# Optimization experiments

Hardware: AMD Instinct MI355X
Metric: run time of the kernel (lower is better)

## Reference

```python
import jax, jax.numpy as jnp
import numpy as np

HIDDEN = 1024
HEADS = 16
HEAD_DIM = HIDDEN // HEADS
LN_EPS = 1e-6


def setup_inputs() -> dict:
    key = jax.random.key(0)
    ks = jax.random.split(key, 12)
    B, S, H = 2, 2048, HIDDEN
    s = 1.0 / np.sqrt(H)
    inp = {
        "hidden_states": jax.random.normal(ks[0], (B, S, H), dtype=jnp.float32),
        "attention_mask": jnp.ones((B, S), dtype=jnp.int32),
        "Wq": jax.random.normal(ks[1], (H, H), dtype=jnp.float32) * s,
        "bq": jax.random.normal(ks[2], (H,), dtype=jnp.float32) * 0.02,
        "Wk": jax.random.normal(ks[3], (H, H), dtype=jnp.float32) * s,
        "bk": jax.random.normal(ks[4], (H,), dtype=jnp.float32) * 0.02,
        "Wv": jax.random.normal(ks[5], (H, H), dtype=jnp.float32) * s,
        "bv": jax.random.normal(ks[6], (H,), dtype=jnp.float32) * 0.02,
        "Wo": jax.random.normal(ks[7], (H, H), dtype=jnp.float32) * s,
        "bo": jax.random.normal(ks[8], (H,), dtype=jnp.float32) * 0.02,
        "ln_g": jnp.ones((H,), dtype=jnp.float32),
        "ln_b": jnp.zeros((H,), dtype=jnp.float32),
    }
    return inp


def _split_heads(x):
    B, S, H = x.shape
    return x.reshape(B, S, HEADS, HEAD_DIM).transpose(0, 2, 1, 3)  # [B,h,S,d]


def reference(hidden_states, attention_mask, Wq, bq, Wk, bk, Wv, bv, Wo, bo, ln_g, ln_b):
    # torch nn.Linear: y = x @ W.T + b
    q = _split_heads(hidden_states @ Wq.T + bq)
    k = _split_heads(hidden_states @ Wk.T + bk)
    v = _split_heads(hidden_states @ Wv.T + bv)

    scores = jnp.einsum("bhqd,bhkd->bhqk", q, k) / np.sqrt(HEAD_DIM)
    # 2D mask path: [B,K] -> [B,1,1,K]; (1-mask)*-1e18 additive bias
    bias = (1.0 - attention_mask[:, None, None, :].astype(scores.dtype)) * -1e18
    probs = jax.nn.softmax(scores + bias, axis=-1)
    # dropout is identity in eval mode
    ctx = jnp.einsum("bhqk,bhkd->bhqd", probs, v)
    B, h, S, d = ctx.shape
    ctx = ctx.transpose(0, 2, 1, 3).reshape(B, S, h * d)

    out = ctx @ Wo.T + bo
    res = out + hidden_states
    mu = jnp.mean(res, axis=-1, keepdims=True)
    var = jnp.mean(jnp.square(res - mu), axis=-1, keepdims=True)
    return (res - mu) * jax.lax.rsqrt(var + LN_EPS) * ln_g + ln_b
```

## Files before the change

kernel.cpp:

```cpp
#include <hip/hip_runtime.h>
#include <hip/hip_bf16.h>

#define SEQ     2048
#define BATCH   2
#define HID     1024
#define NHEADS  16
#define HD      64
#define MTOT    4096
#define KVHALF  1024
#define LNEPS   1e-6f
#define L2E     1.4426950408889634f
#define SHIFT2  26.0f

typedef __bf16 bf16_t;
typedef bf16_t bf16x8 __attribute__((ext_vector_type(8)));
typedef bf16_t bf16x4 __attribute__((ext_vector_type(4)));
typedef short  short4v __attribute__((ext_vector_type(4)));
typedef float  floatx4 __attribute__((ext_vector_type(4)));

__device__ __forceinline__ floatx4 mfma16(bf16x8 a, bf16x8 b, floatx4 c) {
    return __builtin_amdgcn_mfma_f32_16x16x32_bf16(a, b, c, 0, 0, 0);
}
__device__ __forceinline__ floatx4 mfma16k16(bf16x4 a, bf16x4 b, floatx4 c) {
    short4v as = __builtin_bit_cast(short4v, a);
    short4v bs = __builtin_bit_cast(short4v, b);
    return __builtin_amdgcn_mfma_f32_16x16x16bf16_1k(as, bs, c, 0, 0, 0);
}
__device__ __forceinline__ bf16x8 ldg8(const bf16_t* p) { return *(const bf16x8*)p; }

__device__ __forceinline__ void glds16(const bf16_t* src, char* dst) {
    __builtin_amdgcn_global_load_lds(
        (const __attribute__((address_space(1))) unsigned int*)src,
        (__attribute__((address_space(3))) unsigned int*)dst, 16, 0, 0);
}

__device__ __forceinline__ void stage128x32(const bf16_t* __restrict__ g, int row_stride,
                                            int k0, bf16_t* lds, int wave, int lane)
{
#pragma unroll
    for (int j = 0; j < 2; j++) {
        const int rbase = wave * 32 + j * 16;
        const bf16_t* src = g + (size_t)(rbase + (lane >> 2)) * row_stride + k0 + (lane & 3) * 8;
        bf16_t* dst = lds + rbase * 32;
        __builtin_amdgcn_global_load_lds(
            (const __attribute__((address_space(1))) unsigned int*)src,
            (__attribute__((address_space(3))) unsigned int*)dst, 16, 0, 0);
    }
}
__device__ __forceinline__ void stage64x32(const bf16_t* __restrict__ g, int row_stride,
                                           int k0, bf16_t* lds, int wave, int lane)
{
    const int rbase = wave * 16;
    const bf16_t* src = g + (size_t)(rbase + (lane >> 2)) * row_stride + k0 + (lane & 3) * 8;
    bf16_t* dst = lds + rbase * 32;
    __builtin_amdgcn_global_load_lds(
        (const __attribute__((address_space(1))) unsigned int*)src,
        (__attribute__((address_space(3))) unsigned int*)dst, 16, 0, 0);
}

__global__ __launch_bounds__(256) void cvt_kernel(
    const float* sX, const float* sWq, const float* sWk, const float* sWv, const float* sWo,
    bf16_t* dX, bf16_t* dWq, bf16_t* dWk, bf16_t* dWv, bf16_t* dWo)
{
    const int z = blockIdx.z;
    const float* src; bf16_t* dst; int n;
    switch (z) {
        case 0:  src = sX;  dst = dX;  n = MTOT * HID; break;
        case 1:  src = sWq; dst = dWq; n = HID * HID;  break;
        case 2:  src = sWk; dst = dWk; n = HID * HID;  break;
        case 3:  src = sWv; dst = dWv; n = HID * HID;  break;
        default: src = sWo; dst = dWo; n = HID * HID;  break;
    }
    const int n4 = n >> 2;
    const int stride = gridDim.x * blockDim.x;
    for (int i = blockIdx.x * blockDim.x + threadIdx.x; i < n4; i += stride) {
        const float4 v = ((const float4*)src)[i];
        bf16_t o[4] = {(bf16_t)v.x, (bf16_t)v.y, (bf16_t)v.z, (bf16_t)v.w};
        *(unsigned long long*)(dst + 4 * i) = *(unsigned long long*)o;
    }
}

__global__ __launch_bounds__(256) void qkv_kernel(
    const bf16_t* __restrict__ X,
    const bf16_t* __restrict__ Wq, const float* __restrict__ bq,
    const bf16_t* __restrict__ Wk, const float* __restrict__ bk,
    const bf16_t* __restrict__ Wv, const float* __restrict__ bv,
    bf16_t* __restrict__ Qo, bf16_t* __restrict__ Ko, bf16_t* __restrict__ Vo)
{
    const int z = blockIdx.z;
    const bf16_t* W    = (z == 0) ? Wq : (z == 1) ? Wk : Wv;
    const float*  bias = (z == 0) ? bq : (z == 1) ? bk : bv;
    bf16_t*       out  = (z == 0) ? Qo : (z == 1) ? Ko : Vo;

    const int tid  = threadIdx.x;
    const int lane = tid & 63;
    const int wave = tid >> 6;
    const int l16  = lane & 15;
    const int quad = lane >> 4;
    const int m_blk = blockIdx.y * 128;
    const int n_blk = blockIdx.x * 128;
    const int m_w = (wave >> 1) * 64;
    const int n_w = (wave & 1) * 64;

    __shared__ __align__(16) char smem[18432];
    bf16_t* As = (bf16_t*)smem;
    bf16_t* Bs = (bf16_t*)(smem + 8192);

    floatx4 acc[4][4];
#pragma unroll
    for (int i = 0; i < 4; i++)
#pragma unroll
        for (int j = 0; j < 4; j++) acc[i][j] = (floatx4)0.0f;

    for (int k0 = 0; k0 < HID; k0 += 32) {
        __syncthreads();
        stage128x32(X + (size_t)m_blk * HID, HID, k0, As, wave, lane);
        stage128x32(W + (size_t)n_blk * HID, HID, k0, Bs, wave, lane);
        __syncthreads();

        bf16x8 a[4], b[4];
#pragma unroll
        for (int i = 0; i < 4; i++) a[i] = *(const bf16x8*)&As[(m_w + i * 16 + l16) * 32 + quad * 8];
#pragma unroll
        for (int j = 0; j < 4; j++) b[j] = *(const bf16x8*)&Bs[(n_w + j * 16 + l16) * 32 + quad * 8];
#pragma unroll
        for (int i = 0; i < 4; i++)
#pragma unroll
            for (int j = 0; j < 4; j++) acc[i][j] = mfma16(a[i], b[j], acc[i][j]);
    }
    __syncthreads();

    float bv_[4];
#pragma unroll
    for (int j = 0; j < 4; j++) bv_[j] = bias[n_blk + n_w + j * 16 + l16];

    bf16_t* Tw = (bf16_t*)(smem + wave * 4608);

    if (z != 2) {
        const float scale = (z == 0) ? 0.125f : 1.0f;
        const int hN = (n_blk + n_w) >> 6;
#pragma unroll
        for (int ih = 0; ih < 2; ih++) {
#pragma unroll
            for (int i2 = 0; i2 < 2; i2++) {
                const int i = ih * 2 + i2;
#pragma unroll
                for (int j = 0; j < 4; j++)
#pragma unroll
                    for (int r = 0; r < 4; r++)
                        Tw[(i2 * 16 + quad * 4 + r) * 72 + j * 16 + l16] =
                            (bf16_t)((acc[i][j][r] + bv_[j]) * scale);
            }
#pragma unroll
            for (int p = 0; p < 4; p++) {
                const int srow = p * 8 + (lane >> 3);
                const int col  = (lane & 7) * 8;
                bf16x8 v = *(const bf16x8*)&Tw[srow * 72 + col];
                const int m = m_blk + m_w + ih * 32 + srow;
                const int bb = m >> 11, s = m & (SEQ - 1);
                *(bf16x8*)&out[(((size_t)(bb * NHEADS + hN)) * SEQ + s) * HD + col] = v;
            }
        }
    } else {
        const int m0 = m_blk + m_w;
        const int bb = m0 >> 11, s0 = m0 & (SEQ - 1);
#pragma unroll
        for (int jh = 0; jh < 2; jh++) {
#pragma unroll
            for (int j2 = 0; j2 < 2; j2++) {
                const int j = jh * 2 + j2;
#pragma unroll
                for (int i = 0; i < 4; i++) {
                    bf16x4 pk;
#pragma unroll
                    for (int r = 0; r < 4; r++) pk[r] = (bf16_t)(acc[i][j][r] + bv_[j]);
                    *(bf16x4*)&Tw[(j2 * 16 + l16) * 72 + i * 16 + quad * 4] = pk;
                }
            }
#pragma unroll
            for (int p = 0; p < 4; p++) {
                const int srow = p * 8 + (lane >> 3);
                const int col  = (lane & 7) * 8;
                bf16x8 v = *(const bf16x8*)&Tw[srow * 72 + col];
                const int n = n_blk + n_w + jh * 32 + srow;
                const int h = n >> 6, d = n & 63;
                *(bf16x8*)&out[(((size_t)(bb * NHEADS + h)) * HD + d) * SEQ + s0 + col] = v;
            }
        }
    }
}

__global__ __launch_bounds__(512, 4) void attn_kernel(
    const bf16_t* __restrict__ Q, const bf16_t* __restrict__ K,
    const bf16_t* __restrict__ Vt, const int* __restrict__ mask,
    bf16_t* __restrict__ ctx)
{
    const int B   = blockIdx.x;
    const int xcd = B & 7;
    const int idx = B >> 3;
    const int bh  = xcd * 4 + (idx & 3);
    const int q0  = (idx >> 2) * 128;
    const int b   = bh >> 4;
    const int h   = bh & 15;
    const int tid  = threadIdx.x;
    const int wave = tid >> 6;
    const int wq   = wave & 3;
    const int kh   = wave >> 2;
    const int lane = tid & 63;
    const int l16  = lane & 15;
    const int quad = lane >> 4;
    const int r7   = l16 & 7;

    const bf16_t* Qh = Q  + (size_t)bh * SEQ * HD;
    const bf16_t* Kh = K  + (size_t)bh * SEQ * HD;
    const bf16_t* Vh = Vt + (size_t)bh * HD * SEQ;
    const int*    mk = mask + b * SEQ;

    __shared__ __align__(16) char smem[73728];
    char*  base  = smem + kh * 32768;
    char*  Kb0   = base;
    char*  Vb0   = base + 8192;
    char*  Kb1   = base + 16384;
    char*  Vb1   = base + 24576;
    float* bias2 = (float*)(smem + 65536);

    const int qw  = q0 + wq * 32;
    const int kvb = kh * KVHALF;

    const int srow = wq * 8 + (lane >> 3);
    const int cK   = lane & 7;
    const bf16_t* srcK = Kh + (size_t)(kvb + srow) * HD + ((cK ^ (srow & 7)) * 8);
    const bf16_t* srcV = Vh + (size_t)srow * SEQ + kvb + (((2 * cK) ^ (srow & 14)) * 4);
    const int dofs = wq * 1024;

    const int kb0 = l16 * 128 + (((quad    ) ^ r7) << 4);
    const int kb1 = l16 * 128 + (((4 + quad) ^ r7) << 4);

    glds16(srcK,                Kb0 + dofs);
    glds16(srcK + 32 * HD,      Kb0 + dofs + 4096);
    glds16(srcV,                Vb0 + dofs);
    glds16(srcV + 32 * SEQ,     Vb0 + dofs + 4096);
    for (int i = tid; i < SEQ; i += 512)
        bias2[i] = (mk[i] ? 0.0f : -1.0e30f) - SHIFT2;

    bf16x8 bQ[2][2];
#pragma unroll
    for (int qh = 0; qh < 2; qh++)
#pragma unroll
        for (int kc = 0; kc < 2; kc++)
            bQ[qh][kc] = ldg8(Qh + (size_t)(qw + qh * 16 + l16) * HD + kc * 32 + quad * 8);

    const bf16x4 onesA = {(bf16_t)1.0f, (bf16_t)1.0f, (bf16_t)1.0f, (bf16_t)1.0f};
    floatx4 O[2][4];
    floatx4 psA[2];
#pragma unroll
    for (int qh = 0; qh < 2; qh++) {
        psA[qh] = (floatx4)0.0f;
#pragma unroll
        for (int dt = 0; dt < 4; dt++) O[qh][dt] = (floatx4)0.0f;
    }

    __syncthreads();

#define STAGE(kt, KB, VB)                                            \
    do {                                                             \
        const bf16_t* sk_ = srcK + (size_t)(kt) * HD;                \
        const bf16_t* sv_ = srcV + (kt);                             \
        glds16(sk_,            (KB) + dofs);                         \
        glds16(sk_ + 32 * HD,  (KB) + dofs + 4096);                  \
        glds16(sv_,            (VB) + dofs);                         \
        glds16(sv_ + 32 * SEQ, (VB) + dofs + 4096);                  \
    } while (0)

#define COMPUTE(kt, KB, VB)                                                       \
    do {                                                                          \
        __builtin_amdgcn_s_setprio(1);                                            \
        _Pragma("unroll")                                                         \
        for (int kvt = 0; kvt < 4; kvt++) {                                       \
            bf16x8 aK0 = *(const bf16x8*)((KB) + kb0 + kvt * 2048);               \
            bf16x8 aK1 = *(const bf16x8*)((KB) + kb1 + kvt * 2048);               \
            const floatx4 ad = *(const floatx4*)&bias2[kvb + (kt) + kvt * 16 + quad * 4]; \
            bf16x4 pb[2];                                                         \
            _Pragma("unroll")                                                     \
            for (int qh = 0; qh < 2; qh++) {                                      \
                floatx4 s = (floatx4)0.0f;                                        \
                s = mfma16(aK0, bQ[qh][0], s);                                    \
                s = mfma16(aK1, bQ[qh][1], s);                                    \
                floatx4 p;                                                        \
                _Pragma("unroll")                                                 \
                for (int r = 0; r < 4; r++)                                       \
                    p[r] = __builtin_amdgcn_exp2f(fmaf(s[r], L2E, ad[r]));        \
                _Pragma("unroll")                                                 \
                for (int r = 0; r < 4; r++) pb[qh][r] = (bf16_t)p[r];             \
            }                                                                     \
            psA[0] = mfma16k16(onesA, pb[0], psA[0]);                             \
            psA[1] = mfma16k16(onesA, pb[1], psA[1]);                             \
            const int vofs = l16 * 128 + ((((kvt << 2) + quad) ^ (l16 & 14)) << 3); \
            _Pragma("unroll")                                                     \
            for (int dt = 0; dt < 4; dt++) {                                      \
                bf16x4 aV = *(const bf16x4*)((VB) + vofs + dt * 2048);            \
                O[0][dt] = mfma16k16(aV, pb[0], O[0][dt]);                        \
                O[1][dt] = mfma16k16(aV, pb[1], O[1][dt]);                        \
            }                                                                     \
        }                                                                         \
        __builtin_amdgcn_s_setprio(0);                                            \
    } while (0)

    for (int t = 0; t < 16; t += 2) {
        STAGE((t + 1) * 64, Kb1, Vb1);
        COMPUTE(t * 64, Kb0, Vb0);
        __syncthreads();
        if (t + 2 < 16) STAGE((t + 2) * 64, Kb0, Vb0);
        COMPUTE((t + 1) * 64, Kb1, Vb1);
        __syncthreads();
    }
#undef STAGE
#undef COMPUTE

    if (kh == 1) {
        float* mw = (float*)(smem + wq * 10240) + lane * 40;
#pragma unroll
        for (int qh = 0; qh < 2; qh++) {
#pragma unroll
            for (int dt = 0; dt < 4; dt++)
                *(floatx4*)(mw + qh * 16 + dt * 4) = O[qh][dt];
            *(floatx4*)(mw + 32 + qh * 4) = psA[qh];
        }
    }
    __syncthreads();
    if (kh == 1) return;

    {
        const float* mr = (const float*)(smem + wq * 10240) + lane * 40;
#pragma unroll
        for (int qh = 0; qh < 2; qh++) {
#pragma unroll
            for (int dt = 0; dt < 4; dt++)
                O[qh][dt] += *(const floatx4*)(mr + qh * 16 + dt * 4);
            psA[qh] += *(const floatx4*)(mr + 32 + qh * 4);
        }
    }

#pragma unroll
    for (int qh = 0; qh < 2; qh++) {
        const float su = psA[qh][0];
        const float linv = (su > 0.0f) ? 1.0f / su : 0.0f;

        bf16_t* Pw = (bf16_t*)(smem + wq * 10240 + qh * 2304);
#pragma unroll
        for (int dt = 0; dt < 4; dt++) {
            floatx4 o = O[qh][dt] * linv;
            bf16x4 pk;
#pragma unroll
            for (int r = 0; r < 4; r++) pk[r] = (bf16_t)o[r];
            *(bf16x4*)&Pw[l16 * 72 + dt * 16 + quad * 4] = pk;
        }
#pragma unroll
        for (int ch = 0; ch < 2; ch++) {
            const int cc  = ch * 64 + lane;
            const int row = cc >> 3;
            const int col = (cc & 7) * 8;
            bf16x8 vv = *(const bf16x8*)&Pw[row * 72 + col];
            *(bf16x8*)&ctx[((size_t)(b * SEQ + qw + qh * 16 + row)) * HID + h * 64 + col] = vv;
        }
    }
}

__global__ __launch_bounds__(256) void oproj_kernel(
    const bf16_t* __restrict__ C, const bf16_t* __restrict__ Wo,
    const float* __restrict__ bo, const float* __restrict__ X,
    float* __restrict__ res)
{
    const int tid  = threadIdx.x;
    const int lane = tid & 63;
    const int wave = tid >> 6;
    const int l16  = lane & 15;
    const int quad = lane >> 4;
    const int m_blk = blockIdx.y * 64;
    const int n_blk = blockIdx.x * 128;
    const int n_w   = wave * 32;

    __shared__ __align__(16) char smem[12288];
    bf16_t* As = (bf16_t*)smem;
    bf16_t* Bs = (bf16_t*)(smem + 4096);

    floatx4 acc[4][2];
#pragma unroll
    for (int i = 0; i < 4; i++)
#pragma unroll
        for (int j = 0; j < 2; j++) acc[i][j] = (floatx4)0.0f;

    for (int k0 = 0; k0 < HID; k0 += 32) {
        __syncthreads();
        stage64x32 (C  + (size_t)m_blk * HID, HID, k0, As, wave, lane);
        stage128x32(Wo + (size_t)n_blk * HID, HID, k0, Bs, wave, lane);
        __syncthreads();

        bf16x8 a[4], b[2];
#pragma unroll
        for (int i = 0; i < 4; i++) a[i] = *(const bf16x8*)&As[(i * 16 + l16) * 32 + quad * 8];
#pragma unroll
        for (int j = 0; j < 2; j++) b[j] = *(const bf16x8*)&Bs[(n_w + j * 16 + l16) * 32 + quad * 8];
#pragma unroll
        for (int i = 0; i < 4; i++)
#pragma unroll
            for (int j = 0; j < 2; j++) acc[i][j] = mfma16(a[i], b[j], acc[i][j]);
    }
    __syncthreads();

    float bv_[2];
#pragma unroll
    for (int j = 0; j < 2; j++) bv_[j] = bo[n_blk + n_w + j * 16 + l16];

    float* Tw = (float*)(smem + wave * 2304);
#pragma unroll
    for (int ch = 0; ch < 4; ch++) {
#pragma unroll
        for (int j = 0; j < 2; j++)
#pragma unroll
            for (int r = 0; r < 4; r++)
                Tw[(quad * 4 + r) * 36 + j * 16 + l16] = acc[ch][j][r] + bv_[j];
#pragma unroll
        for (int cc = 0; cc < 2; cc++) {
            const int idx = cc * 64 + lane;
            const int row = idx >> 3;
            const int col = (idx & 7) * 4;
            float4 v = *(const float4*)&Tw[row * 36 + col];
            const int m = m_blk + ch * 16 + row;
            const float4 xv = *(const float4*)&X[(size_t)m * HID + n_blk + n_w + col];
            v.x += xv.x; v.y += xv.y; v.z += xv.z; v.w += xv.w;
            *(float4*)&res[(size_t)m * HID + n_blk + n_w + col] = v;
        }
    }
}

__global__ __launch_bounds__(256) void ln_kernel(
    const float* __restrict__ res,
    const float* __restrict__ g, const float* __restrict__ be,
    float* __restrict__ out)
{
    __shared__ float red1[4], red2[4];
    const int row  = blockIdx.x;
    const int lane = threadIdx.x & 63;
    const int wave = threadIdx.x >> 6;
    const float4 v = ((const float4*)(res + (size_t)row * HID))[threadIdx.x];

    float s = v.x + v.y + v.z + v.w;
#pragma unroll
    for (int off = 1; off < 64; off <<= 1) s += __shfl_xor(s, off, 64);
    if (lane == 0) red1[wave] = s;
    __syncthreads();
    const float mu = (red1[0] + red1[1] + red1[2] + red1[3]) * (1.0f / HID);

    const float d0 = v.x - mu, d1 = v.y - mu, d2 = v.z - mu, d3 = v.w - mu;
    float ss = d0 * d0 + d1 * d1 + d2 * d2 + d3 * d3;
#pragma unroll
    for (int off = 1; off < 64; off <<= 1) ss += __shfl_xor(ss, off, 64);
    if (lane == 0) red2[wave] = ss;
    __syncthreads();
    const float var = (red2[0] + red2[1] + red2[2] + red2[3]) * (1.0f / HID);
    const float rstd = rsqrtf(var + LNEPS);

    const float4 gv = ((const float4*)g)[threadIdx.x];
    const float4 bv = ((const float4*)be)[threadIdx.x];
    float4 o;
    o.x = d0 * rstd * gv.x + bv.x;
    o.y = d1 * rstd * gv.y + bv.y;
    o.z = d2 * rstd * gv.z + bv.z;
    o.w = d3 * rstd * gv.w + bv.w;
    ((float4*)(out + (size_t)row * HID))[threadIdx.x] = o;
}

extern "C" void kernel_launch(void* const* d_in, const int* in_sizes, int n_in,
                              void* d_out, int out_size, void* d_ws, size_t ws_size,
                              hipStream_t stream)
{
    const float* X  = (const float*)d_in[0];
    const int* mask = (const int*)d_in[1];
    const float* Wq = (const float*)d_in[2];  const float* bq = (const float*)d_in[3];
    const float* Wk = (const float*)d_in[4];  const float* bk = (const float*)d_in[5];
    const float* Wv = (const float*)d_in[6];  const float* bv = (const float*)d_in[7];
    const float* Wo = (const float*)d_in[8];  const float* bo = (const float*)d_in[9];
    const float* g  = (const float*)d_in[10]; const float* be = (const float*)d_in[11];
    float* out = (float*)d_out;

    char* ws = (char*)d_ws;
    bf16_t* Qb  = (bf16_t*)(ws);
    bf16_t* Kb  = (bf16_t*)(ws + (8ull  << 20));
    bf16_t* Vb  = (bf16_t*)(ws + (16ull << 20));
    bf16_t* Cb  = (bf16_t*)(ws + (24ull << 20));
    float*  Rb  = (float*)(ws);
    bf16_t* Xc  = (bf16_t*)(ws + (32ull << 20));
    bf16_t* Wqc = (bf16_t*)(ws + (40ull << 20));
    bf16_t* Wkc = (bf16_t*)(ws + (42ull << 20));
    bf16_t* Wvc = (bf16_t*)(ws + (44ull << 20));
    bf16_t* Woc = (bf16_t*)(ws + (46ull << 20));

    cvt_kernel <<<dim3(128, 1, 5), 256, 0, stream>>>(X, Wq, Wk, Wv, Wo, Xc, Wqc, Wkc, Wvc, Woc);
    qkv_kernel <<<dim3(8, 32, 3), 256, 0, stream>>>(Xc, Wqc, bq, Wkc, bk, Wvc, bv, Qb, Kb, Vb);
    attn_kernel<<<dim3(512), 512, 0, stream>>>(Qb, Kb, Vb, mask, Cb);
    oproj_kernel<<<dim3(8, 64), 256, 0, stream>>>(Cb, Woc, bo, X, Rb);
    ln_kernel  <<<MTOT, 256, 0, stream>>>(Rb, g, be, out);
}
```

Before: 125.0 us.

## Double K-step to 64 and XOR-swizzle LDS tiles in QKV and O-proj GEMMs

The QKV and output-projection GEMM loops now stage 64-wide K slices instead of 32, which halves the number of barrier pairs per tile. Global-to-LDS loads are placed in an XOR-swizzled layout (chunk index xor row&7) with 128-byte rows, and fragment reads apply the matching swizzle. The aim is to cut synchronization overhead and LDS bank conflicts on the 16-byte fragment reads. In exchange, LDS use per block doubles, which could lower occupancy.

```diff
diff --git a/kernel.cpp b/kernel.cpp
--- a/kernel.cpp
+++ b/kernel.cpp
@@ -34,28 +34,18 @@
         (__attribute__((address_space(3))) unsigned int*)dst, 16, 0, 0);
 }
 
-__device__ __forceinline__ void stage128x32(const bf16_t* __restrict__ g, int row_stride,
-                                            int k0, bf16_t* lds, int wave, int lane)
-{
-#pragma unroll
-    for (int j = 0; j < 2; j++) {
-        const int rbase = wave * 32 + j * 16;
-        const bf16_t* src = g + (size_t)(rbase + (lane >> 2)) * row_stride + k0 + (lane & 3) * 8;
-        bf16_t* dst = lds + rbase * 32;
-        __builtin_amdgcn_global_load_lds(
-            (const __attribute__((address_space(1))) unsigned int*)src,
-            (__attribute__((address_space(3))) unsigned int*)dst, 16, 0, 0);
-    }
-}
-__device__ __forceinline__ void stage64x32(const bf16_t* __restrict__ g, int row_stride,
-                                           int k0, bf16_t* lds, int wave, int lane)
-{
-    const int rbase = wave * 16;
-    const bf16_t* src = g + (size_t)(rbase + (lane >> 2)) * row_stride + k0 + (lane & 3) * 8;
-    bf16_t* dst = lds + rbase * 32;
-    __builtin_amdgcn_global_load_lds(
-        (const __attribute__((address_space(1))) unsigned int*)src,
-        (__attribute__((address_space(3))) unsigned int*)dst, 16, 0, 0);
+__device__ __forceinline__ void stage8_sw(const bf16_t* __restrict__ gtile, int stride,
+                                          int k0, bf16_t* lds, int rbase, int lane)
+{
+    const int row = rbase + (lane >> 3);
+    const int c8  = lane & 7;
+    const bf16_t* src = gtile + (size_t)row * stride + k0 + (((c8 ^ (row & 7))) << 3);
+    glds16(src, (char*)lds + rbase * 128);
+}
+
+__device__ __forceinline__ bf16x8 frag_sw(const bf16_t* lds, int R, int ks, int quad, int r7)
+{
+    return *(const bf16x8*)((const char*)lds + R * 128 + ((((ks << 2) + quad) ^ r7) << 4));
 }
 
 __global__ __launch_bounds__(256) void cvt_kernel(
@@ -97,14 +87,18 @@
     const int wave = tid >> 6;
     const int l16  = lane & 15;
     const int quad = lane >> 4;
+    const int r7   = l16 & 7;
     const int m_blk = blockIdx.y * 128;
     const int n_blk = blockIdx.x * 128;
     const int m_w = (wave >> 1) * 64;
     const int n_w = (wave & 1) * 64;
 
-    __shared__ __align__(16) char smem[18432];
+    const bf16_t* Xt = X + (size_t)m_blk * HID;
+    const bf16_t* Wt = W + (size_t)n_blk * HID;
+
+    __shared__ __align__(16) char smem[32768];
     bf16_t* As = (bf16_t*)smem;
-    bf16_t* Bs = (bf16_t*)(smem + 8192);
+    bf16_t* Bs = (bf16_t*)(smem + 16384);
 
     floatx4 acc[4][4];
 #pragma unroll
@@ -112,21 +106,27 @@
 #pragma unroll
         for (int j = 0; j < 4; j++) acc[i][j] = (floatx4)0.0f;
 
-    for (int k0 = 0; k0 < HID; k0 += 32) {
+    for (int k0 = 0; k0 < HID; k0 += 64) {
         __syncthreads();
-        stage128x32(X + (size_t)m_blk * HID, HID, k0, As, wave, lane);
-        stage128x32(W + (size_t)n_blk * HID, HID, k0, Bs, wave, lane);
+#pragma unroll
+        for (int j = 0; j < 4; j++) {
+            stage8_sw(Xt, HID, k0, As, wave * 32 + j * 8, lane);
+            stage8_sw(Wt, HID, k0, Bs, wave * 32 + j * 8, lane);
+        }
         __syncthreads();
 
-        bf16x8 a[4], b[4];
-#pragma unroll
-        for (int i = 0; i < 4; i++) a[i] = *(const bf16x8*)&As[(m_w + i * 16 + l16) * 32 + quad * 8];
-#pragma unroll
-        for (int j = 0; j < 4; j++) b[j] = *(const bf16x8*)&Bs[(n_w + j * 16 + l16) * 32 + quad * 8];
-#pragma unroll
-        for (int i = 0; i < 4; i++)
-#pragma unroll
-            for (int j = 0; j < 4; j++) acc[i][j] = mfma16(a[i], b[j], acc[i][j]);
+#pragma unroll
+        for (int ks = 0; ks < 2; ks++) {
+            bf16x8 a[4], b[4];
+#pragma unroll
+            for (int i = 0; i < 4; i++) a[i] = frag_sw(As, m_w + i * 16 + l16, ks, quad, r7);
+#pragma unroll
+            for (int j = 0; j < 4; j++) b[j] = frag_sw(Bs, n_w + j * 16 + l16, ks, quad, r7);
+#pragma unroll
+            for (int i = 0; i < 4; i++)
+#pragma unroll
+                for (int j = 0; j < 4; j++) acc[i][j] = mfma16(a[i], b[j], acc[i][j]);
+        }
     }
     __syncthreads();
 
@@ -376,13 +376,17 @@
     const int wave = tid >> 6;
     const int l16  = lane & 15;
     const int quad = lane >> 4;
+    const int r7   = l16 & 7;
     const int m_blk = blockIdx.y * 64;
     const int n_blk = blockIdx.x * 128;
     const int n_w   = wave * 32;
 
-    __shared__ __align__(16) char smem[12288];
+    const bf16_t* Ct = C  + (size_t)m_blk * HID;
+    const bf16_t* Wt = Wo + (size_t)n_blk * HID;
+
+    __shared__ __align__(16) char smem[24576];
     bf16_t* As = (bf16_t*)smem;
-    bf16_t* Bs = (bf16_t*)(smem + 4096);
+    bf16_t* Bs = (bf16_t*)(smem + 8192);
 
     floatx4 acc[4][2];
 #pragma unroll
@@ -390,21 +394,28 @@
 #pragma unroll
         for (int j = 0; j < 2; j++) acc[i][j] = (floatx4)0.0f;
 
-    for (int k0 = 0; k0 < HID; k0 += 32) {
+    for (int k0 = 0; k0 < HID; k0 += 64) {
         __syncthreads();
-        stage64x32 (C  + (size_t)m_blk * HID, HID, k0, As, wave, lane);
-        stage128x32(Wo + (size_t)n_blk * HID, HID, k0, Bs, wave, lane);
+#pragma unroll
+        for (int j = 0; j < 2; j++)
+            stage8_sw(Ct, HID, k0, As, wave * 16 + j * 8, lane);
+#pragma unroll
+        for (int j = 0; j < 4; j++)
+            stage8_sw(Wt, HID, k0, Bs, wave * 32 + j * 8, lane);
         __syncthreads();
 
-        bf16x8 a[4], b[2];
-#pragma unroll
-        for (int i = 0; i < 4; i++) a[i] = *(const bf16x8*)&As[(i * 16 + l16) * 32 + quad * 8];
-#pragma unroll
-        for (int j = 0; j < 2; j++) b[j] = *(const bf16x8*)&Bs[(n_w + j * 16 + l16) * 32 + quad * 8];
-#pragma unroll
-        for (int i = 0; i < 4; i++)
-#pragma unroll
-            for (int j = 0; j < 2; j++) acc[i][j] = mfma16(a[i], b[j], acc[i][j]);
+#pragma unroll
+        for (int ks = 0; ks < 2; ks++) {
+            bf16x8 a[4], b[2];
+#pragma unroll
+            for (int i = 0; i < 4; i++) a[i] = frag_sw(As, i * 16 + l16, ks, quad, r7);
+#pragma unroll
+            for (int j = 0; j < 2; j++) b[j] = frag_sw(Bs, n_w + j * 16 + l16, ks, quad, r7);
+#pragma unroll
+            for (int i = 0; i < 4; i++)
+#pragma unroll
+                for (int j = 0; j < 2; j++) acc[i][j] = mfma16(a[i], b[j], acc[i][j]);
+        }
     }
     __syncthreads();
 
```

Measured after the change: 131.6 us. 5.3% more time.
